# Optimization experiments

Measured on AMD Instinct MI355X. Metric: run time of the kernel, lower is better.

## Reference

```python
import jax, jax.numpy as jnp
import numpy as np

GENE_NUM = 3000
N_NODES = 50000
N_EDGES = 1000000
DIM = 128


def setup_inputs() -> dict:
    key = jax.random.key(0)
    ks = jax.random.split(key, 8)
    h = jax.random.normal(ks[0], (N_NODES, DIM), dtype=jnp.float32)
    alpha = jax.random.normal(ks[1], (GENE_NUM + 2,), dtype=jnp.float32)
    edge_weight = jax.random.uniform(ks[2], (N_EDGES,), dtype=jnp.float32)
    # Xavier-uniform Linear weight, zero bias
    gain = float(np.sqrt(2.0))  # calculate_gain('relu')
    bound = gain * np.sqrt(6.0 / (DIM + DIM))
    W = jax.random.uniform(ks[3], (DIM, DIM), minval=-bound, maxval=bound, dtype=jnp.float32)
    b = jnp.zeros((DIM,), dtype=jnp.float32)
    # node ids: genes 0..GENE_NUM-1 have id = gene index (>=0); cells have id = -1 (<0)
    node_id = jnp.concatenate([
        jnp.arange(GENE_NUM, dtype=jnp.int64),
        -jnp.ones((N_NODES - GENE_NUM,), dtype=jnp.int64),
    ])
    edge_src = jax.random.randint(ks[4], (N_EDGES,), 0, N_NODES, dtype=jnp.int64)
    edge_dst = jax.random.randint(ks[5], (N_EDGES,), 0, N_NODES, dtype=jnp.int64)
    return {"h": h, "alpha": alpha, "edge_weight": edge_weight, "W": W, "b": b,
            "node_id": node_id, "edge_src": edge_src, "edge_dst": edge_dst}


def reference(h, alpha, edge_weight, W, b, node_id, edge_src, edge_dst):
    gene_num = alpha.shape[0] - 2
    src_id = node_id[edge_src]  # [E]
    dst_id = node_id[edge_dst]  # [E]
    # default: cell self-loop alpha -> index gene_num + 1
    idx = jnp.full(edge_src.shape, gene_num + 1, dtype=jnp.int32)
    idx = jnp.where((src_id >= 0) & (dst_id < 0), src_id.astype(jnp.int32), idx)   # gene->cell: beta[src]
    idx = jnp.where((dst_id >= 0) & (src_id < 0), dst_id.astype(jnp.int32), idx)   # cell->gene: beta[dst]
    idx = jnp.where((dst_id >= 0) & (src_id >= 0), gene_num, idx)                  # gene self-loop alpha
    # gather -> per-edge message [E, D]
    coeff = alpha[idx] * edge_weight                     # [E]
    msg = h[edge_src] * coeff[:, None]                   # [E, D]
    # scatter-mean over destination nodes
    n = h.shape[0]
    summ = jax.ops.segment_sum(msg, edge_dst, num_segments=n)           # [N, D]
    cnt = jax.ops.segment_sum(jnp.ones_like(edge_weight), edge_dst, num_segments=n)
    neigh = summ / jnp.maximum(cnt, 1.0)[:, None]
    # MLP: dropout(eval, identity) -> Linear -> ReLU -> norm(identity)
    z = jax.nn.relu(neigh @ W.T + b)
    return z
```

## Files before the change

### kernel.cpp

```cpp
#include <hip/hip_runtime.h>

#define D 128
#define PSHIFT 6
#define PSIZE 64
#define EDGES_PER_BLK 4096
#define CAP 2048
#define MAXPART 1024

typedef __attribute__((ext_vector_type(8))) short bf16x8;
typedef __attribute__((ext_vector_type(4))) float f32x4;

__device__ __forceinline__ unsigned short f2bf(float f) {
  unsigned int u = __float_as_uint(f);
  u = (u + 0x7fffu + ((u >> 16) & 1)) >> 16;
  return (unsigned short)u;
}

__global__ __launch_bounds__(512) void cvt_hist_kernel(
    const float* __restrict__ h, unsigned short* __restrict__ h16, int total4,
    const int* __restrict__ edst, int* __restrict__ g_hist, int E,
    int cvtBlocks) {
  if ((int)blockIdx.x < cvtBlocks) {
    int i = blockIdx.x * 512 + threadIdx.x;
    if (i >= total4) return;
    float4 v = ((const float4*)h)[i];
    ushort4 o;
    o.x = f2bf(v.x); o.y = f2bf(v.y); o.z = f2bf(v.z); o.w = f2bf(v.w);
    ((ushort4*)h16)[i] = o;
    return;
  }
  __shared__ int cnt[MAXPART];
  int t = threadIdx.x;
  cnt[t] = 0; cnt[t + 512] = 0;
  __syncthreads();
  int eb = (blockIdx.x - cvtBlocks) * EDGES_PER_BLK;
#pragma unroll
  for (int q = 0; q < 8; ++q) {
    int e = eb + q * 512 + t;
    if (e < E) atomicAdd(&cnt[edst[e] >> PSHIFT], 1);
  }
  __syncthreads();
  int c = cnt[t];
  if (c > 0) atomicAdd(&g_hist[t], c);
  c = cnt[t + 512];
  if (c > 0) atomicAdd(&g_hist[t + 512], c);
}

__global__ __launch_bounds__(512) void part_scan_kernel(
    const int* __restrict__ g_hist, int* __restrict__ part_off,
    int* __restrict__ g_cursor, int E, int npart) {
  __shared__ int ts[512];
  int t = threadIdx.x;
  int i0 = 2 * t, i1 = 2 * t + 1;
  int v0 = (i0 < npart) ? g_hist[i0] : 0;
  int v1 = (i1 < npart) ? g_hist[i1] : 0;
  ts[t] = v0 + v1;
  __syncthreads();
  for (int off = 1; off < 512; off <<= 1) {
    int x = (t >= off) ? ts[t - off] : 0;
    __syncthreads();
    ts[t] += x;
    __syncthreads();
  }
  int excl = ts[t] - (v0 + v1);
  if (i0 < npart) { part_off[i0] = excl; g_cursor[i0] = excl; }
  if (i1 < npart) { part_off[i1] = excl + v0; g_cursor[i1] = excl + v0; }
  if (t == 0) part_off[npart] = E;
}

__global__ __launch_bounds__(512) void bin_scatter_kernel(
    const float* __restrict__ alpha, const float* __restrict__ ew,
    const int* __restrict__ node_id, const int* __restrict__ esrc,
    const int* __restrict__ edst, int* __restrict__ g_cursor,
    int2* __restrict__ recs, int E, int gene_num) {
  __shared__ int2 lrec[EDGES_PER_BLK];
  __shared__ unsigned short lbin[EDGES_PER_BLK];
  __shared__ int cnt[MAXPART], offl[MAXPART], gbase[MAXPART];
  __shared__ int ts[512];

  int t = threadIdx.x;
  cnt[t] = 0; cnt[t + 512] = 0;
  __syncthreads();

  int eb = blockIdx.x * EDGES_PER_BLK;
  int rx[8]; float rc[8]; int rb[8]; int rk[8];
#pragma unroll
  for (int q = 0; q < 8; ++q) {
    int e = eb + q * 512 + t;
    rk[q] = -1;
    if (e < E) {
      int src = esrc[e];
      int dst = edst[e];
      int sid = node_id[src];
      int did = node_id[dst];
      int idx;
      if (sid >= 0) idx = (did >= 0) ? gene_num : sid;
      else          idx = (did >= 0) ? did : (gene_num + 1);
      rc[q] = alpha[idx] * ew[e];
      rx[q] = src | ((dst & (PSIZE - 1)) << 16);
      int b = dst >> PSHIFT;
      rb[q] = b;
      rk[q] = atomicAdd(&cnt[b], 1);
    }
  }
  __syncthreads();

  int c0 = cnt[2 * t], c1 = cnt[2 * t + 1];
  ts[t] = c0 + c1;
  __syncthreads();
  for (int off = 1; off < 512; off <<= 1) {
    int x = (t >= off) ? ts[t - off] : 0;
    __syncthreads();
    ts[t] += x;
    __syncthreads();
  }
  int exclp = ts[t] - (c0 + c1);
  offl[2 * t] = exclp;
  offl[2 * t + 1] = exclp + c0;
  __syncthreads();

#pragma unroll
  for (int q = 0; q < 8; ++q) {
    if (rk[q] >= 0) {
      int ls = offl[rb[q]] + rk[q];
      lrec[ls] = make_int2(rx[q], __float_as_int(rc[q]));
      lbin[ls] = (unsigned short)rb[q];
    }
  }
  __syncthreads();

  {
    int c = cnt[t];
    if (c > 0) gbase[t] = atomicAdd(&g_cursor[t], c);
    c = cnt[t + 512];
    if (c > 0) gbase[t + 512] = atomicAdd(&g_cursor[t + 512], c);
  }
  __syncthreads();

  int tot = E - eb;
  if (tot > EDGES_PER_BLK) tot = EDGES_PER_BLK;
  for (int s = t; s < tot; s += 512) {
    int b = lbin[s];
    recs[gbase[b] + (s - offl[b])] = lrec[s];
  }
}

__global__ __launch_bounds__(512) void part_acc_kernel(
    const unsigned short* __restrict__ h16, const int2* __restrict__ recs,
    const int* __restrict__ part_off, float* __restrict__ neigh, int N) {
  __shared__ int2 lrec[CAP];
  __shared__ int cnt[PSIZE], offl[PSIZE];

  int t = threadIdx.x;
  int p = blockIdx.x;
  if (t < PSIZE) cnt[t] = 0;
  __syncthreads();

  int start = part_off[p];
  int R = part_off[p + 1] - start;
  if (R > CAP) R = CAP;

  int2 rq[4]; int dlq[4]; int rkq[4];
#pragma unroll
  for (int q = 0; q < 4; ++q) {
    int s = q * 512 + t;
    rkq[q] = -1;
    if (s < R) {
      int2 r = recs[start + s];
      rq[q] = r;
      int dl = (r.x >> 16) & (PSIZE - 1);
      dlq[q] = dl;
      rkq[q] = atomicAdd(&cnt[dl], 1);
    }
  }
  __syncthreads();

  if (t < PSIZE) offl[t] = cnt[t];
  __syncthreads();
  for (int off = 1; off < PSIZE; off <<= 1) {
    int x = 0;
    if (t < PSIZE && t >= off) x = offl[t - off];
    __syncthreads();
    if (t < PSIZE) offl[t] += x;
    __syncthreads();
  }
  if (t < PSIZE) offl[t] -= cnt[t];
  __syncthreads();

#pragma unroll
  for (int q = 0; q < 4; ++q)
    if (rkq[q] >= 0) lrec[offl[dlq[q]] + rkq[q]] = rq[q];
  __syncthreads();

  int w = t >> 6;
  int l = t & 63;
  const unsigned int* hp = ((const unsigned int*)h16) + l;

  for (int dd = 0; dd < 4; ++dd) {
    int dlA = w * 8 + 2 * dd;
    int dlB = dlA + 1;
    int cA = cnt[dlA], oA = offl[dlA];
    int cB = cnt[dlB], oB = offl[dlB];
    float axA = 0.f, ayA = 0.f, axB = 0.f, ayB = 0.f;
    int cmax = (cA > cB) ? cA : cB;
    for (int k = 0; k < cmax; k += 8) {
      float cfA[8], cfB[8];
      unsigned int vA[8], vB[8];
      int aA[8], aB[8];
#pragma unroll
      for (int q = 0; q < 8; ++q) {
        int2 rA = lrec[oA + k + q];
        int2 rB = lrec[oB + k + q];
        bool okA = (k + q) < cA;
        bool okB = (k + q) < cB;
        aA[q] = okA ? (rA.x & 0xffff) : 0;
        aB[q] = okB ? (rB.x & 0xffff) : 0;
        cfA[q] = okA ? __int_as_float(rA.y) : 0.f;
        cfB[q] = okB ? __int_as_float(rB.y) : 0.f;
      }
#pragma unroll
      for (int q = 0; q < 8; ++q) {
        vA[q] = hp[(size_t)aA[q] * 64];
        vB[q] = hp[(size_t)aB[q] * 64];
      }
#pragma unroll
      for (int q = 0; q < 8; ++q) {
        axA += cfA[q] * __uint_as_float(vA[q] << 16);
        ayA += cfA[q] * __uint_as_float(vA[q] & 0xffff0000u);
        axB += cfB[q] * __uint_as_float(vB[q] << 16);
        ayB += cfB[q] * __uint_as_float(vB[q] & 0xffff0000u);
      }
    }
    int dstA = p * PSIZE + dlA;
    int dstB = p * PSIZE + dlB;
    if (dstA < N) {
      float inv = 1.0f / (float)(cA > 0 ? cA : 1);
      ((float2*)neigh)[(size_t)dstA * (D / 2) + l] =
          make_float2(axA * inv, ayA * inv);
    }
    if (dstB < N) {
      float inv = 1.0f / (float)(cB > 0 ? cB : 1);
      ((float2*)neigh)[(size_t)dstB * (D / 2) + l] =
          make_float2(axB * inv, ayB * inv);
    }
  }
}

__global__ __launch_bounds__(256) void mlp_mfma_kernel(
    const float* __restrict__ W, const float* __restrict__ bias,
    float* __restrict__ io, int N) {
  __shared__ __align__(16) unsigned short Wl[128 * 128];

  int t = threadIdx.x;
#pragma unroll
  for (int i = 0; i < 8; ++i) {
    int chunk = t + 256 * i;
    int row = chunk >> 4;
    int cb = chunk & 15;
    const float* gp = W + (size_t)row * 128 + cb * 8;
    float4 a = *(const float4*)gp;
    float4 b = *(const float4*)(gp + 4);
    bf16x8 v;
    v[0] = (short)f2bf(a.x); v[1] = (short)f2bf(a.y);
    v[2] = (short)f2bf(a.z); v[3] = (short)f2bf(a.w);
    v[4] = (short)f2bf(b.x); v[5] = (short)f2bf(b.y);
    v[6] = (short)f2bf(b.z); v[7] = (short)f2bf(b.w);
    *(bf16x8*)((char*)Wl + row * 256 + ((cb ^ (row & 7)) << 4)) = v;
  }
  __syncthreads();

  int l = t & 63;
  int w = t >> 6;
  int kg = l >> 4;
  int m_base = blockIdx.x * 64 + w * 16;
  int arow = m_base + (l & 15);
  if (arow >= N) arow = N - 1;

  bf16x8 af[4];
  const float* ap = io + (size_t)arow * 128 + kg * 8;
#pragma unroll
  for (int kk = 0; kk < 4; ++kk) {
    float4 a = *(const float4*)(ap + kk * 32);
    float4 b = *(const float4*)(ap + kk * 32 + 4);
    bf16x8 v;
    v[0] = (short)f2bf(a.x); v[1] = (short)f2bf(a.y);
    v[2] = (short)f2bf(a.z); v[3] = (short)f2bf(a.w);
    v[4] = (short)f2bf(b.x); v[5] = (short)f2bf(b.y);
    v[6] = (short)f2bf(b.z); v[7] = (short)f2bf(b.w);
    af[kk] = v;
  }

#pragma unroll
  for (int c = 0; c < 8; ++c) {
    f32x4 acc = {0.f, 0.f, 0.f, 0.f};
    int row_w = c * 16 + (l & 15);
    int rs = row_w & 7;
#pragma unroll
    for (int kk = 0; kk < 4; ++kk) {
      int cb = kk * 4 + kg;
      bf16x8 bf = *(bf16x8*)((char*)Wl + row_w * 256 + ((cb ^ rs) << 4));
      acc = __builtin_amdgcn_mfma_f32_16x16x32_bf16(af[kk], bf, acc, 0, 0, 0);
    }
    int j = c * 16 + (l & 15);
    float bj = bias[j];
#pragma unroll
    for (int r = 0; r < 4; ++r) {
      int m = m_base + kg * 4 + r;
      if (m < N) io[(size_t)m * 128 + j] = fmaxf(acc[r] + bj, 0.0f);
    }
  }
}

extern "C" void kernel_launch(void* const* d_in, const int* in_sizes, int n_in,
                              void* d_out, int out_size, void* d_ws, size_t ws_size,
                              hipStream_t stream) {
  const float* h     = (const float*)d_in[0];
  const float* alpha = (const float*)d_in[1];
  const float* ew    = (const float*)d_in[2];
  const float* W     = (const float*)d_in[3];
  const float* bias  = (const float*)d_in[4];
  const int* node_id = (const int*)d_in[5];
  const int* esrc    = (const int*)d_in[6];
  const int* edst    = (const int*)d_in[7];
  float* out = (float*)d_out;

  int E = in_sizes[2];
  int N = in_sizes[5];
  int gene_num = in_sizes[1] - 2;
  int npart = (N + PSIZE - 1) / PSIZE;
  int eblocks = (E + EDGES_PER_BLK - 1) / EDGES_PER_BLK;
  int total4 = N * D / 4;
  int cvtBlocks = (total4 + 511) / 512;

  int* g_hist   = (int*)d_ws;
  int* part_off = g_hist + MAXPART;
  int* g_cursor = part_off + MAXPART + 1;
  size_t h16_off = ((size_t)(3 * MAXPART + 1) * sizeof(int) + 15) & ~(size_t)15;
  unsigned short* h16 = (unsigned short*)((char*)d_ws + h16_off);
  size_t rec_off = (h16_off + (size_t)N * D * sizeof(unsigned short) + 15) & ~(size_t)15;
  int2* recs = (int2*)((char*)d_ws + rec_off);
  size_t need = rec_off + (size_t)E * sizeof(int2);
  if (ws_size < need) return;

  hipMemsetAsync(g_hist, 0, MAXPART * sizeof(int), stream);

  cvt_hist_kernel<<<cvtBlocks + eblocks, 512, 0, stream>>>(
      h, h16, total4, edst, g_hist, E, cvtBlocks);
  part_scan_kernel<<<1, 512, 0, stream>>>(g_hist, part_off, g_cursor, E, npart);
  bin_scatter_kernel<<<eblocks, 512, 0, stream>>>(alpha, ew, node_id, esrc,
                                                  edst, g_cursor, recs, E,
                                                  gene_num);
  part_acc_kernel<<<npart, 512, 0, stream>>>(h16, recs, part_off, out, N);
  {
    int blocks = (N + 63) / 64;
    mlp_mfma_kernel<<<blocks, 256, 0, stream>>>(W, bias, out, N);
  }
}
```

Before: 115.7 us.

## Split feature dim into four chunks with chunked bf16 layout for gather locality

The bf16 copy of h is rewritten in a chunk-major layout, with 32 features per chunk, and the accumulation kernel launches four blocks per partition, each covering one chunk. Within a wave, 16 lanes cover the feature pairs and 4 lanes split the edges, and partial sums are combined with xor shuffles. The aim is a smaller per-chunk gather footprint that fits cache better, plus more blocks for parallelism. In exchange, every chunk block redoes the record load and local sort, and only a quarter of the lanes write output.

```diff
diff --git a/kernel.cpp b/kernel.cpp
--- a/kernel.cpp
+++ b/kernel.cpp
@@ -6,6 +6,7 @@
 #define EDGES_PER_BLK 4096
 #define CAP 2048
 #define MAXPART 1024
+#define NCHUNK 4
 
 typedef __attribute__((ext_vector_type(8))) short bf16x8;
 typedef __attribute__((ext_vector_type(4))) float f32x4;
@@ -19,14 +20,19 @@
 __global__ __launch_bounds__(512) void cvt_hist_kernel(
     const float* __restrict__ h, unsigned short* __restrict__ h16, int total4,
     const int* __restrict__ edst, int* __restrict__ g_hist, int E,
-    int cvtBlocks) {
+    int cvtBlocks, int N) {
   if ((int)blockIdx.x < cvtBlocks) {
     int i = blockIdx.x * 512 + threadIdx.x;
     if (i >= total4) return;
     float4 v = ((const float4*)h)[i];
     ushort4 o;
     o.x = f2bf(v.x); o.y = f2bf(v.y); o.z = f2bf(v.z); o.w = f2bf(v.w);
-    ((ushort4*)h16)[i] = o;
+    int f = i * 4;
+    int n = f >> 7;
+    int d = f & 127;
+    int c = d >> 5;
+    int wi = d & 31;
+    ((ushort4*)h16)[(size_t)c * N * 8 + n * 8 + (wi >> 2)] = o;
     return;
   }
   __shared__ int cnt[MAXPART];
@@ -152,7 +158,8 @@
   __shared__ int cnt[PSIZE], offl[PSIZE];
 
   int t = threadIdx.x;
-  int p = blockIdx.x;
+  int p = blockIdx.x >> 2;
+  int chunk = blockIdx.x & 3;
   if (t < PSIZE) cnt[t] = 0;
   __syncthreads();
 
@@ -194,7 +201,9 @@
 
   int w = t >> 6;
   int l = t & 63;
-  const unsigned int* hp = ((const unsigned int*)h16) + l;
+  int esub = l >> 4;
+  int dpair = l & 15;
+  const unsigned int* hp = ((const unsigned int*)h16) + (size_t)chunk * N * 16 + dpair;
 
   for (int dd = 0; dd < 4; ++dd) {
     int dlA = w * 8 + 2 * dd;
@@ -203,45 +212,55 @@
     int cB = cnt[dlB], oB = offl[dlB];
     float axA = 0.f, ayA = 0.f, axB = 0.f, ayB = 0.f;
     int cmax = (cA > cB) ? cA : cB;
-    for (int k = 0; k < cmax; k += 8) {
-      float cfA[8], cfB[8];
-      unsigned int vA[8], vB[8];
-      int aA[8], aB[8];
-#pragma unroll
-      for (int q = 0; q < 8; ++q) {
-        int2 rA = lrec[oA + k + q];
-        int2 rB = lrec[oB + k + q];
-        bool okA = (k + q) < cA;
-        bool okB = (k + q) < cB;
+    for (int k = 0; k < cmax; k += 16) {
+      float cfA[4], cfB[4];
+      unsigned int vA[4], vB[4];
+      int aA[4], aB[4];
+#pragma unroll
+      for (int q = 0; q < 4; ++q) {
+        int sl = k + 4 * q + esub;
+        int iA = oA + sl; iA = (iA < CAP) ? iA : (CAP - 1);
+        int iB = oB + sl; iB = (iB < CAP) ? iB : (CAP - 1);
+        int2 rA = lrec[iA];
+        int2 rB = lrec[iB];
+        bool okA = sl < cA;
+        bool okB = sl < cB;
         aA[q] = okA ? (rA.x & 0xffff) : 0;
         aB[q] = okB ? (rB.x & 0xffff) : 0;
         cfA[q] = okA ? __int_as_float(rA.y) : 0.f;
         cfB[q] = okB ? __int_as_float(rB.y) : 0.f;
       }
 #pragma unroll
-      for (int q = 0; q < 8; ++q) {
-        vA[q] = hp[(size_t)aA[q] * 64];
-        vB[q] = hp[(size_t)aB[q] * 64];
-      }
-#pragma unroll
-      for (int q = 0; q < 8; ++q) {
+      for (int q = 0; q < 4; ++q) {
+        vA[q] = hp[(size_t)aA[q] * 16];
+        vB[q] = hp[(size_t)aB[q] * 16];
+      }
+#pragma unroll
+      for (int q = 0; q < 4; ++q) {
         axA += cfA[q] * __uint_as_float(vA[q] << 16);
         ayA += cfA[q] * __uint_as_float(vA[q] & 0xffff0000u);
         axB += cfB[q] * __uint_as_float(vB[q] << 16);
         ayB += cfB[q] * __uint_as_float(vB[q] & 0xffff0000u);
       }
     }
+    axA += __shfl_xor(axA, 16); ayA += __shfl_xor(ayA, 16);
+    axB += __shfl_xor(axB, 16); ayB += __shfl_xor(ayB, 16);
+    axA += __shfl_xor(axA, 32); ayA += __shfl_xor(ayA, 32);
+    axB += __shfl_xor(axB, 32); ayB += __shfl_xor(ayB, 32);
+
     int dstA = p * PSIZE + dlA;
     int dstB = p * PSIZE + dlB;
-    if (dstA < N) {
-      float inv = 1.0f / (float)(cA > 0 ? cA : 1);
-      ((float2*)neigh)[(size_t)dstA * (D / 2) + l] =
-          make_float2(axA * inv, ayA * inv);
-    }
-    if (dstB < N) {
-      float inv = 1.0f / (float)(cB > 0 ? cB : 1);
-      ((float2*)neigh)[(size_t)dstB * (D / 2) + l] =
-          make_float2(axB * inv, ayB * inv);
+    if (l < 16) {
+      if (dstA < N) {
+        float inv = 1.0f / (float)(cA > 0 ? cA : 1);
+        ((float2*)neigh)[(size_t)dstA * 64 + chunk * 16 + dpair] =
+            make_float2(axA * inv, ayA * inv);
+      }
+      if (dstB < N) {
+        float inv = 1.0f / (float)(cB > 0 ? cB : 1);
+        ((float2*)neigh)[(size_t)dstB * 64 + chunk * 16 + dpair] =
+            make_float2(axB * inv, ayB * inv);
+      }
     }
   }
 }
@@ -345,12 +364,12 @@
   hipMemsetAsync(g_hist, 0, MAXPART * sizeof(int), stream);
 
   cvt_hist_kernel<<<cvtBlocks + eblocks, 512, 0, stream>>>(
-      h, h16, total4, edst, g_hist, E, cvtBlocks);
+      h, h16, total4, edst, g_hist, E, cvtBlocks, N);
   part_scan_kernel<<<1, 512, 0, stream>>>(g_hist, part_off, g_cursor, E, npart);
   bin_scatter_kernel<<<eblocks, 512, 0, stream>>>(alpha, ew, node_id, esrc,
                                                   edst, g_cursor, recs, E,
                                                   gene_num);
-  part_acc_kernel<<<npart, 512, 0, stream>>>(h16, recs, part_off, out, N);
+  part_acc_kernel<<<npart * NCHUNK, 512, 0, stream>>>(h16, recs, part_off, out, N);
   {
     int blocks = (N + 63) / 64;
     mlp_mfma_kernel<<<blocks, 256, 0, stream>>>(W, bias, out, N);
```

Result: no change. 117.8 us (+1.8%).
